# Kernel tuning notes

Measured on AMD Instinct MI355X. Metric: run time of the kernel, lower is better.

The kernel has to match this reference:

```python
import jax, jax.numpy as jnp
import numpy as np

K_BINS = 2048
EMB = 64
MU = 0.99
THRESHOLD = 1.0


def setup_inputs() -> dict:
    key = jax.random.key(0)
    kx, kk = jax.random.split(key)
    x = jax.random.normal(kx, (131072, EMB), dtype=jnp.float32)
    k = jax.random.normal(kk, (K_BINS, EMB), dtype=jnp.float32)
    # restore_k semantics: k_sum starts as a copy of k, k_elem as ones
    return {"x": x, "k": k, "k_sum": k, "k_elem": jnp.ones((K_BINS,), jnp.float32)}


def reference(x, k, k_sum, k_elem):
    N, T = x.shape  # T == EMB (preprocess branch 1)
    # preprocess: prenorm statistic
    prenorm = jnp.linalg.norm(x - jnp.mean(x)) / np.sqrt(x.size)

    # quantise: squared-L2 distance to codebook, argmin, fit
    dist = (jnp.sum(x * x, axis=-1, keepdims=True)
            - 2.0 * (x @ k.T)
            + jnp.sum(k * k, axis=-1)[None, :])  # (N, K_BINS)
    x_l = jnp.argmin(dist, axis=-1)               # (N,)
    fit = jnp.mean(jnp.min(dist, axis=-1))

    # dequantise: codebook gather
    x_d = k[x_l]                                  # (N, EMB)

    # update_k (torch.no_grad block): EMA codebook update
    _k_sum = jax.ops.segment_sum(x, x_l, num_segments=K_BINS)          # == onehot @ x
    _k_elem = jax.ops.segment_sum(jnp.ones((N,), x.dtype), x_l, num_segments=K_BINS)
    # N >= K_BINS so _tile is identity; randperm -> deterministic jax perm
    perm = jax.random.permutation(jax.random.key(42), N)
    _k_rand = x[perm[:K_BINS]]                    # (K_BINS, EMB)
    new_k_sum = MU * k_sum + (1.0 - MU) * _k_sum
    new_k_elem = MU * k_elem + (1.0 - MU) * _k_elem
    usage = (new_k_elem[:, None] >= THRESHOLD).astype(x.dtype)
    new_k = usage * (new_k_sum / new_k_elem[:, None]) + (1.0 - usage) * _k_rand
    _k_prob = _k_elem / jnp.sum(_k_elem)
    entropy = -jnp.sum(_k_prob * jnp.log(_k_prob + 1e-8))
    used_curr = jnp.sum((_k_elem >= THRESHOLD).astype(jnp.int32))
    usage_total = jnp.sum(usage)
    dk = jnp.linalg.norm(new_k - k) / np.sqrt(new_k.size)

    # commit loss (x_d detached) and straight-through estimator
    commit_loss = jnp.sum((jax.lax.stop_gradient(x_d) - x) ** 2) / x.size
    x_d_st = x + jax.lax.stop_gradient(x_d - x)

    # postprocess: view(N, T, -1).permute(0, 2, 1) -> (N, 1, EMB)
    x_d_out = x_d_st.reshape(N, T, -1).transpose(0, 2, 1)
    return (x_l, x_d_out, commit_loss, fit, prenorm,
            entropy, used_curr, usage_total, dk,
            new_k, new_k_sum, new_k_elem)
```

## Files before the change

kernel.cpp:

```cpp
#include <hip/hip_runtime.h>
#include <stdint.h>

#define N_ROWS 131072
#define DIM 64
#define KB 2048
#define M_ELEMS 8388608

#define O_XL   0
#define O_XD   131072
#define O_CL   8519680
#define O_FIT  8519681
#define O_PRE  8519682
#define O_ENT  8519683
#define O_USED 8519684
#define O_UTOT 8519685
#define O_DK   8519686
#define O_NK   8519687
#define O_NKS  8650759
#define O_NKE  8781831

#define A_DBL   0
#define A_CNT   64
#define A_KK2N  128
#define A_KST   8320
#define A_XLI   532608
#define A_KCNT  1056896
#define A_BCUR  1065088
#define A_KRAND 1073280
#define A_BOFF  1597568
#define A_FLAG  1605760
#define A_ROWL  2130048
#define A_KS64  2654336
#define A_BITS  1605760
#define A_PKEY  2130048
#define A_HIST  3702912
#define A_BSUM  3833984
#define A_CUR   3834496
#define A_PIDX  3965568
#define A_RES1  4489856
#define WS_END  5014144

typedef short bf16x8 __attribute__((ext_vector_type(8)));
typedef float f32x4 __attribute__((ext_vector_type(4)));

#define GLL16(G, L) __builtin_amdgcn_global_load_lds( \
    (const __attribute__((address_space(1))) void*)(G), \
    (__attribute__((address_space(3))) void*)(L), 16, 0, 0)
#define GLL4(G, L) __builtin_amdgcn_global_load_lds( \
    (const __attribute__((address_space(1))) void*)(G), \
    (__attribute__((address_space(3))) void*)(L), 4, 0, 0)


__device__ __forceinline__ float block_reduce_sum(float v, float* lds) {
  #pragma unroll
  for (int off = 32; off > 0; off >>= 1) v += __shfl_down(v, off, 64);
  int lane = threadIdx.x & 63, wid = threadIdx.x >> 6;
  if (lane == 0) lds[wid] = v;
  __syncthreads();
  float r = 0.f;
  if (threadIdx.x == 0) {
    int nw = blockDim.x >> 6;
    for (int i = 0; i < nw; ++i) r += lds[i];
  }
  __syncthreads();
  return r;
}

__device__ __forceinline__ unsigned short f2bf_rne(float f) {
  uint32_t u = __float_as_uint(f);
  uint32_t r = u + 0x7FFFu + ((u >> 16) & 1u);
  return (unsigned short)(r >> 16);
}

#define TF_ROUND(r) do { x0 += x1; x1 = (x1 << (r)) | (x1 >> (32 - (r))); x1 ^= x0; } while (0)

__device__ __forceinline__ void threefry2x32(uint32_t k0, uint32_t k1,
                                             uint32_t c0, uint32_t c1,
                                             uint32_t& o0, uint32_t& o1) {
  uint32_t k2 = k0 ^ k1 ^ 0x1BD11BDAu;
  uint32_t x0 = c0 + k0, x1 = c1 + k1;
  TF_ROUND(13); TF_ROUND(15); TF_ROUND(26); TF_ROUND(6);
  x0 += k1; x1 += k2 + 1u;
  TF_ROUND(17); TF_ROUND(29); TF_ROUND(16); TF_ROUND(24);
  x0 += k2; x1 += k0 + 2u;
  TF_ROUND(13); TF_ROUND(15); TF_ROUND(26); TF_ROUND(6);
  x0 += k0; x1 += k1 + 3u;
  TF_ROUND(17); TF_ROUND(29); TF_ROUND(16); TF_ROUND(24);
  x0 += k1; x1 += k2 + 4u;
  TF_ROUND(13); TF_ROUND(15); TF_ROUND(26); TF_ROUND(6);
  x0 += k2; x1 += k0 + 5u;
  o0 = x0; o1 = x1;
}

__global__ __launch_bounds__(256) void k_prep(
    const float* __restrict__ k, unsigned short* __restrict__ kst,
    float* __restrict__ kk2n) {
  int w = (blockIdx.x * blockDim.x + threadIdx.x) >> 6;
  int lane = threadIdx.x & 63;
  float v = k[(size_t)w * DIM + lane];
  unsigned short h = f2bf_rne(v);
  float hf = __uint_as_float((uint32_t)h << 16);
  unsigned short lo = f2bf_rne(v - hf);
  int t = w >> 4, r = w & 15;
  int c = lane >> 3, e = lane & 7;
  int slot = c ^ (r & 7);
  size_t u16i = (size_t)t * 2048 + r * 64 + slot * 8 + e;
  kst[u16i] = h;
  kst[u16i + 1024] = lo;
  float q = v * v;
  #pragma unroll
  for (int off = 32; off > 0; off >>= 1) q += __shfl_down(q, off, 64);
  if (lane == 0) kk2n[w] = -0.5f * q;
}

__global__ __launch_bounds__(512) void k_main(
    const float* __restrict__ x, const unsigned short* __restrict__ kst,
    const float* __restrict__ kk2n,
    int* __restrict__ xli, uint32_t* __restrict__ flag, int* __restrict__ cnt,
    double* __restrict__ dbl) {
  __shared__ __align__(16) char smem[8704];
  __shared__ float lds_red[8];
  int lane = threadIdx.x & 63;
  int wid = threadIdx.x >> 6;
  int lrow = lane & 15;
  int lk = lane >> 4;
  int r0 = (blockIdx.x * 8 + wid) * 32;

  bf16x8 xh[2][2], xl[2][2];
  float s_acc = 0.f, q_acc = 0.f;
  #pragma unroll
  for (int g = 0; g < 2; ++g) {
    #pragma unroll
    for (int kt = 0; kt < 2; ++kt) {
      const float* xp = x + (size_t)(r0 + g * 16 + lrow) * DIM + kt * 32 + lk * 8;
      float4 v0 = *(const float4*)xp;
      float4 v1 = *(const float4*)(xp + 4);
      float vv[8] = {v0.x, v0.y, v0.z, v0.w, v1.x, v1.y, v1.z, v1.w};
      #pragma unroll
      for (int i = 0; i < 8; ++i) {
        float v = vv[i];
        s_acc += v;
        q_acc = fmaf(v, v, q_acc);
        unsigned short h = f2bf_rne(v);
        float hf = __uint_as_float((uint32_t)h << 16);
        xh[g][kt][i] = (short)h;
        xl[g][kt][i] = (short)f2bf_rne(v - hf);
      }
    }
  }
  float bs = block_reduce_sum(s_acc, lds_red);
  float bq = block_reduce_sum(q_acc, lds_red);
  if (threadIdx.x == 0) {
    atomicAdd(&dbl[0], (double)bs);
    atomicAdd(&dbl[1], (double)bq);
  }

  int offH0 = lrow * 128 + (((lk    ) ^ (lrow & 7)) << 4);
  int offH1 = lrow * 128 + (((lk + 4) ^ (lrow & 7)) << 4);

  const char* kst_b = (const char*)kst;
  const char* kk_b  = (const char*)kk2n;

  if (wid < 4) GLL16(kst_b + (size_t)wid * 1024 + (size_t)lane * 16, smem + wid * 1024);
  else if (wid == 4) GLL4(kk_b + (size_t)(lane & 15) * 4, smem + 4096);

  float b1[2], b2[2];
  uint32_t j1[2];
  #pragma unroll
  for (int g = 0; g < 2; ++g) { b1[g] = -3.402823466e38f; b2[g] = -3.402823466e38f; j1[g] = 0; }

  for (int t = 0; t < KB / 16; ++t) {
    char* B  = smem + (t & 1) * 4352;
    char* Bn = smem + ((t + 1) & 1) * 4352;
    if (t + 1 < KB / 16) {
      if (wid < 4)
        GLL16(kst_b + (size_t)(t + 1) * 4096 + (size_t)wid * 1024 + (size_t)lane * 16,
              Bn + wid * 1024);
      else if (wid == 4)
        GLL4(kk_b + (size_t)(t + 1) * 64 + (size_t)(lane & 15) * 4, Bn + 4096);
    }
    __syncthreads();

    bf16x8 ah0 = *(const bf16x8*)(B + offH0);
    bf16x8 ah1 = *(const bf16x8*)(B + offH1);
    bf16x8 al0 = *(const bf16x8*)(B + 2048 + offH0);
    bf16x8 al1 = *(const bf16x8*)(B + 2048 + offH1);
    f32x4 kkv  = *(const f32x4*)(B + 4096 + lk * 16);
    uint32_t jb = (uint32_t)(t * 16 + lk * 4);
    #pragma unroll
    for (int g = 0; g < 2; ++g) {
      f32x4 acc = __builtin_amdgcn_mfma_f32_16x16x32_bf16(ah0, xh[g][0], kkv, 0, 0, 0);
      acc = __builtin_amdgcn_mfma_f32_16x16x32_bf16(ah1, xh[g][1], acc, 0, 0, 0);
      acc = __builtin_amdgcn_mfma_f32_16x16x32_bf16(al0, xh[g][0], acc, 0, 0, 0);
      acc = __builtin_amdgcn_mfma_f32_16x16x32_bf16(al1, xh[g][1], acc, 0, 0, 0);
      acc = __builtin_amdgcn_mfma_f32_16x16x32_bf16(ah0, xl[g][0], acc, 0, 0, 0);
      acc = __builtin_amdgcn_mfma_f32_16x16x32_bf16(ah1, xl[g][1], acc, 0, 0, 0);
      #pragma unroll
      for (int reg = 0; reg < 4; ++reg) {
        float v = acc[reg];
        bool gt = v > b1[g];
        float mn = fminf(v, b1[g]);
        b2[g] = fmaxf(b2[g], mn);
        b1[g] = gt ? v : b1[g];
        j1[g] = gt ? (jb + (uint32_t)reg) : j1[g];
      }
    }
    __syncthreads();
  }

  #pragma unroll
  for (int g = 0; g < 2; ++g) {
    #pragma unroll
    for (int s = 16; s <= 32; s <<= 1) {
      float ob1 = __shfl_xor(b1[g], s, 64);
      float ob2 = __shfl_xor(b2[g], s, 64);
      uint32_t oj1 = __shfl_xor(j1[g], s, 64);
      bool gt = ob1 > b1[g];
      float mn = fminf(b1[g], ob1);
      b2[g] = fmaxf(fmaxf(b2[g], ob2), mn);
      b1[g] = fmaxf(b1[g], ob1);
      j1[g] = gt ? oj1 : j1[g];
    }
    if (lk == 0) {
      int row = r0 + g * 16 + lrow;
      xli[row] = (int)j1[g];
      if (b1[g] - b2[g] < 0.01f) {
        int i = atomicAdd(cnt, 1);
        flag[i] = (uint32_t)row;
      }
    }
  }
}

__global__ __launch_bounds__(256) void k_rescan(
    const uint32_t* __restrict__ flag, const int* __restrict__ cnt,
    const float* __restrict__ x, const float* __restrict__ k,
    int* __restrict__ xli) {
  __shared__ float xs[4][64];
  int lane = threadIdx.x & 63;
  int wid = threadIdx.x >> 6;
  int gw = (blockIdx.x * blockDim.x + threadIdx.x) >> 6;
  int n = *cnt;
  for (int fi = gw; fi < n; fi += 1024) {
    int row = flag[fi];
    xs[wid][lane] = x[(size_t)row * DIM + lane];
    double bd = 1e300;
    int bj = 0;
    for (int j = lane; j < KB; j += 64) {
      const float* kr = k + (size_t)j * DIM;
      double e = 0.0;
      #pragma unroll
      for (int d = 0; d < DIM; ++d) {
        double diff = (double)xs[wid][d] - (double)kr[d];
        e = fma(diff, diff, e);
      }
      if (e < bd) { bd = e; bj = j; }
    }
    #pragma unroll
    for (int off = 32; off > 0; off >>= 1) {
      double od = __shfl_down(bd, off, 64);
      int oj = __shfl_down(bj, off, 64);
      if (od < bd || (od == bd && oj < bj)) { bd = od; bj = oj; }
    }
    if (lane == 0) xli[row] = bj;
  }
}

__global__ void k_hist_rows(const int* __restrict__ xli, int* __restrict__ kcnt) {
  int i = blockIdx.x * blockDim.x + threadIdx.x;
  atomicAdd(&kcnt[xli[i]], 1);
}

__global__ __launch_bounds__(256) void k_finish(
    const float* __restrict__ x, const float* __restrict__ k,
    const int* __restrict__ xli, float* __restrict__ out,
    double* __restrict__ dbl) {
  __shared__ float lds[8];
  int row = blockIdx.x * blockDim.x + threadIdx.x;
  int j = xli[row];
  out[O_XL + row] = (float)j;
  const float4* xp = (const float4*)(x + (size_t)row * DIM);
  const float4* kp = (const float4*)(k + (size_t)j * DIM);
  float4* xd = (float4*)(out + O_XD + (size_t)row * DIM);
  float a = 0.f, b = 0.f, c = 0.f, d = 0.f;
  #pragma unroll
  for (int q = 0; q < 16; ++q) {
    float4 kv = kp[q];
    float4 xv = xp[q];
    xd[q] = kv;
    float dx = kv.x - xv.x, dy = kv.y - xv.y;
    float dz = kv.z - xv.z, dw = kv.w - xv.w;
    a = fmaf(dx, dx, a); b = fmaf(dy, dy, b);
    c = fmaf(dz, dz, c); d = fmaf(dw, dw, d);
  }
  float cl = (a + b) + (c + d);
  float bc = block_reduce_sum(cl, lds);
  if (threadIdx.x == 0) atomicAdd(&dbl[2], (double)bc);
}


__global__ __launch_bounds__(1024) void k_scan_bins(const int* __restrict__ kcnt,
                                                    uint32_t* __restrict__ boffs) {
  __shared__ uint32_t part[1024];
  int tid = threadIdx.x;
  uint32_t c0 = (uint32_t)kcnt[2 * tid];
  uint32_t c1 = (uint32_t)kcnt[2 * tid + 1];
  part[tid] = c0 + c1;
  __syncthreads();
  for (int off = 1; off < 1024; off <<= 1) {
    uint32_t v = (tid >= off) ? part[tid - off] : 0u;
    __syncthreads();
    part[tid] += v;
    __syncthreads();
  }
  uint32_t run = (tid > 0) ? part[tid - 1] : 0u;
  boffs[2 * tid] = run;
  boffs[2 * tid + 1] = run + c0;
}

__global__ void k_scatter_rows(const int* __restrict__ xli, const uint32_t* __restrict__ boffs,
                               uint32_t* __restrict__ bcur, uint32_t* __restrict__ rowlist) {
  int i = blockIdx.x * blockDim.x + threadIdx.x;
  int b = xli[i];
  uint32_t pos = boffs[b] + atomicAdd(&bcur[b], 1u);
  rowlist[pos] = (uint32_t)i;
}

__global__ __launch_bounds__(256) void k_segsum(
    const uint32_t* __restrict__ rowlist, const int* __restrict__ xli,
    const float* __restrict__ x, double* __restrict__ ks64) {
  int gw = (blockIdx.x * blockDim.x + threadIdx.x) >> 6;
  int lane = threadIdx.x & 63;
  uint32_t p0 = (uint32_t)gw * 16;
  double acc = 0.0;
  int cur = -1;
  #pragma unroll 4
  for (int i = 0; i < 16; ++i) {
    uint32_t row = rowlist[p0 + i];
    int bin = xli[row];
    if (bin != cur) {
      if (cur >= 0) atomicAdd(&ks64[(size_t)cur * DIM + lane], acc);
      acc = 0.0; cur = bin;
    }
    acc += (double)x[(size_t)row * DIM + lane];
  }
  if (cur >= 0) atomicAdd(&ks64[(size_t)cur * DIM + lane], acc);
}


__global__ void k_bits_hist(int which, uint32_t* __restrict__ bits,
                            uint32_t* __restrict__ hist) {
  uint32_t a0, a1, b0, b1;
  threefry2x32(0u, 42u, 0u, 2u, a0, b0);
  threefry2x32(0u, 42u, 1u, 3u, a1, b1);
  uint32_t k0, k1;
  if (which == 0) { k0 = b0; k1 = b1; }
  else {
    uint32_t c0, c1, d0, d1;
    threefry2x32(a0, a1, 0u, 2u, c0, d0);
    threefry2x32(a0, a1, 1u, 3u, c1, d1);
    k0 = d0; k1 = d1;
  }
  int i = blockIdx.x * blockDim.x + threadIdx.x;
  uint32_t y0, y1;
  threefry2x32(k0, k1, (uint32_t)i, (uint32_t)(i + 65536), y0, y1);
  bits[i] = y0;
  bits[i + 65536] = y1;
  atomicAdd(&hist[y0 >> 17], 1u);
  atomicAdd(&hist[y1 >> 17], 1u);
}

__global__ __launch_bounds__(256) void k_scanA(uint32_t* __restrict__ hist,
                                               uint32_t* __restrict__ bsum) {
  __shared__ uint32_t sh[256];
  int tid = threadIdx.x;
  int bin = blockIdx.x * 256 + tid;
  uint32_t v = hist[bin];
  sh[tid] = v;
  __syncthreads();
  for (int off = 1; off < 256; off <<= 1) {
    uint32_t t = (tid >= off) ? sh[tid - off] : 0u;
    __syncthreads();
    sh[tid] += t;
    __syncthreads();
  }
  hist[bin] = sh[tid] - v;
  if (tid == 255) bsum[blockIdx.x] = sh[tid];
}

__global__ void k_scanB(uint32_t* __restrict__ bsum) {
  __shared__ uint32_t sh[128];
  int tid = threadIdx.x;
  uint32_t v = bsum[tid];
  sh[tid] = v;
  __syncthreads();
  for (int off = 1; off < 128; off <<= 1) {
    uint32_t t = (tid >= off) ? sh[tid - off] : 0u;
    __syncthreads();
    sh[tid] += t;
    __syncthreads();
  }
  bsum[tid] = sh[tid] - v;
}

__global__ void k_scatter(const uint32_t* __restrict__ bits, const uint32_t* __restrict__ hist,
                          const uint32_t* __restrict__ bsum, uint32_t* __restrict__ cursor,
                          uint32_t* __restrict__ pkey, uint32_t* __restrict__ pidx) {
  int i = blockIdx.x * blockDim.x + threadIdx.x;
  uint32_t key = bits[i];
  uint32_t bin = key >> 17;
  uint32_t pos = hist[bin] + bsum[bin >> 8] + atomicAdd(&cursor[bin], 1u);
  pkey[pos] = key; pidx[pos] = (uint32_t)i;
}

__global__ void k_rank(const uint32_t* __restrict__ pkey, const uint32_t* __restrict__ pidx,
                       const uint32_t* __restrict__ hist, const uint32_t* __restrict__ bsum,
                       const uint32_t* __restrict__ cursor,
                       const uint32_t* __restrict__ srcvals, uint32_t* __restrict__ outv,
                       const float* __restrict__ x, float* __restrict__ krand,
                       int limit) {
  int s = blockIdx.x * blockDim.x + threadIdx.x;
  uint32_t myk = pkey[s], myi = pidx[s];
  uint32_t bin = myk >> 17;
  uint32_t start = hist[bin] + bsum[bin >> 8], cntb = cursor[bin];
  uint32_t r = 0;
  for (uint32_t t = 0; t < cntb; ++t) {
    uint32_t ok = pkey[start + t], oi = pidx[start + t];
    r += (ok < myk || (ok == myk && oi < myi)) ? 1u : 0u;
  }
  uint32_t pos = start + r;
  if (limit == 0) {
    outv[pos] = myi;
  } else if (pos < (uint32_t)limit) {
    uint32_t orig = srcvals[myi];
    const float4* xs = (const float4*)(x + (size_t)orig * DIM);
    float4* kd = (float4*)(krand + (size_t)pos * DIM);
    #pragma unroll
    for (int q = 0; q < 16; ++q) kd[q] = xs[q];
  }
}


__global__ __launch_bounds__(256) void k_elem_kernel(
    const double* __restrict__ ks64, const int* __restrict__ kcnt,
    const float* __restrict__ k_sum_in, const float* __restrict__ k_elem_in,
    const float* __restrict__ k_in, const float* __restrict__ krand,
    float* __restrict__ out, double* __restrict__ dbl) {
  __shared__ float lds[8];
  const float OMF = (float)(1.0 - 0.99);
  int e = blockIdx.x * blockDim.x + threadIdx.x;
  int b = e >> 6;
  float part = (float)ks64[e];
  float nks = 0.99f * k_sum_in[e] + OMF * part;
  out[O_NKS + e] = nks;
  float cnt = (float)kcnt[b];
  float ke = 0.99f * k_elem_in[b] + OMF * cnt;
  float nk = (ke >= 1.f) ? (nks / ke) : krand[e];
  out[O_NK + e] = nk;
  float dd = nk - k_in[e];
  float bsum = block_reduce_sum(dd * dd, lds);
  if (threadIdx.x == 0) atomicAdd(&dbl[4], (double)bsum);
}

__global__ __launch_bounds__(1024) void k_finale(
    const int* __restrict__ kcnt, const float* __restrict__ k_elem_in,
    float* __restrict__ out, const double* __restrict__ dbl) {
  __shared__ float ent_l[1024];
  __shared__ int u1_l[1024], u2_l[1024];
  const float OMF = (float)(1.0 - 0.99);
  int tid = threadIdx.x;
  float ent = 0.f; int used = 0, usage = 0;
  #pragma unroll
  for (int t = 0; t < 2; ++t) {
    int b = tid + t * 1024;
    float cnt = (float)kcnt[b];
    float ke = 0.99f * k_elem_in[b] + OMF * cnt;
    out[O_NKE + b] = ke;
    float p = cnt * (1.f / 131072.f);
    ent -= p * logf(p + 1e-8f);
    used += (cnt >= 1.f) ? 1 : 0;
    usage += (ke >= 1.f) ? 1 : 0;
  }
  ent_l[tid] = ent; u1_l[tid] = used; u2_l[tid] = usage;
  __syncthreads();
  for (int off = 512; off > 0; off >>= 1) {
    if (tid < off) {
      ent_l[tid] += ent_l[tid + off];
      u1_l[tid] += u1_l[tid + off];
      u2_l[tid] += u2_l[tid + off];
    }
    __syncthreads();
  }
  if (tid == 0) {
    double M = (double)M_ELEMS;
    double sumS = dbl[0], sumQ = dbl[1];
    double var = (sumQ - sumS * sumS / M) / M;
    out[O_PRE] = (float)sqrt(var > 0.0 ? var : 0.0);
    out[O_FIT] = (float)(dbl[2] / (double)N_ROWS);
    out[O_CL]  = (float)(dbl[2] / M);
    out[O_DK]  = (float)sqrt(dbl[4] / (double)(KB * DIM));
    out[O_ENT] = ent_l[0];
    out[O_USED] = (float)u1_l[0];
    out[O_UTOT] = (float)u2_l[0];
  }
}


extern "C" void kernel_launch(void* const* d_in, const int* in_sizes, int n_in,
                              void* d_out, int out_size, void* d_ws, size_t ws_size,
                              hipStream_t stream) {
  (void)in_sizes; (void)n_in; (void)out_size; (void)ws_size;
  const float* x      = (const float*)d_in[0];
  const float* k      = (const float*)d_in[1];
  const float* k_sum  = (const float*)d_in[2];
  const float* k_elem = (const float*)d_in[3];
  float* out = (float*)d_out;
  char* ws = (char*)d_ws;

  double*   dbl   = (double*)(ws + A_DBL);
  int*      cnt   = (int*)(ws + A_CNT);
  float*    kk2n  = (float*)(ws + A_KK2N);
  unsigned short* kst = (unsigned short*)(ws + A_KST);
  int*      xli   = (int*)(ws + A_XLI);
  int*      kcnt  = (int*)(ws + A_KCNT);
  uint32_t* bcur  = (uint32_t*)(ws + A_BCUR);
  float*    krand = (float*)(ws + A_KRAND);
  uint32_t* boffs = (uint32_t*)(ws + A_BOFF);
  uint32_t* flag  = (uint32_t*)(ws + A_FLAG);
  uint32_t* rowl  = (uint32_t*)(ws + A_ROWL);
  double*   ks64  = (double*)(ws + A_KS64);
  uint32_t* bits  = (uint32_t*)(ws + A_BITS);
  uint32_t* pkey  = (uint32_t*)(ws + A_PKEY);
  uint32_t* hist  = (uint32_t*)(ws + A_HIST);
  uint32_t* bsum  = (uint32_t*)(ws + A_BSUM);
  uint32_t* cur   = (uint32_t*)(ws + A_CUR);
  uint32_t* pidx  = (uint32_t*)(ws + A_PIDX);
  uint32_t* res1  = (uint32_t*)(ws + A_RES1);

  (void)hipMemsetAsync(ws + A_DBL, 0, 128, stream);
  (void)hipMemsetAsync(ws + A_KCNT, 0, 16384, stream);
  (void)hipMemsetAsync(ws + A_KS64, 0, 1048576, stream);

  k_prep<<<512, 256, 0, stream>>>(k, kst, kk2n);
  k_main<<<512, 512, 0, stream>>>(x, kst, kk2n, xli, flag, cnt, dbl);
  k_rescan<<<256, 256, 0, stream>>>(flag, cnt, x, k, xli);
  k_finish<<<512, 256, 0, stream>>>(x, k, xli, out, dbl);

  k_hist_rows<<<512, 256, 0, stream>>>(xli, kcnt);
  k_scan_bins<<<1, 1024, 0, stream>>>(kcnt, boffs);
  k_scatter_rows<<<512, 256, 0, stream>>>(xli, boffs, bcur, rowl);
  k_segsum<<<2048, 256, 0, stream>>>(rowl, xli, x, ks64);

  (void)hipMemsetAsync(ws + A_HIST, 0, 262656, stream);
  k_bits_hist<<<256, 256, 0, stream>>>(0, bits, hist);
  k_scanA<<<128, 256, 0, stream>>>(hist, bsum);
  k_scanB<<<1, 128, 0, stream>>>(bsum);
  k_scatter<<<512, 256, 0, stream>>>(bits, hist, bsum, cur, pkey, pidx);
  k_rank<<<512, 256, 0, stream>>>(pkey, pidx, hist, bsum, cur, nullptr, res1,
                                  nullptr, nullptr, 0);
  (void)hipMemsetAsync(ws + A_HIST, 0, 262656, stream);
  k_bits_hist<<<256, 256, 0, stream>>>(1, bits, hist);
  k_scanA<<<128, 256, 0, stream>>>(hist, bsum);
  k_scanB<<<1, 128, 0, stream>>>(bsum);
  k_scatter<<<512, 256, 0, stream>>>(bits, hist, bsum, cur, pkey, pidx);
  k_rank<<<512, 256, 0, stream>>>(pkey, pidx, hist, bsum, cur, res1, nullptr,
                                  x, krand, 2048);

  k_elem_kernel<<<512, 256, 0, stream>>>(ks64, kcnt, k_sum, k_elem, k, krand, out, dbl);
  k_finale<<<1, 1024, 0, stream>>>(kcnt, k_elem, out, dbl);
}
```

Measured before the change: 392.5 us.

## Enlarge k_main row tile per wave and stage 64 codebook entries per sync

The main distance/argmin kernel now runs 4 waves of 64 rows each (instead of 8 waves of 32 rows) and loads 64 codebook entries per LDS stage instead of 16. Fewer barriers are needed (one per 64 codes), each LDS fragment read is reused across four row groups, and the work per block stays the same. In exchange each wave holds twice as many x fragments and argmin trackers, which raises register pressure and may lower occupancy. The LDS buffer also grows to about 33KB.

```diff
diff --git a/kernel.cpp b/kernel.cpp
--- a/kernel.cpp
+++ b/kernel.cpp
@@ -113,23 +113,24 @@
   if (lane == 0) kk2n[w] = -0.5f * q;
 }
 
-__global__ __launch_bounds__(512) void k_main(
+__global__ __launch_bounds__(256) void k_main(
     const float* __restrict__ x, const unsigned short* __restrict__ kst,
     const float* __restrict__ kk2n,
     int* __restrict__ xli, uint32_t* __restrict__ flag, int* __restrict__ cnt,
     double* __restrict__ dbl) {
-  __shared__ __align__(16) char smem[8704];
-  __shared__ float lds_red[8];
-  int lane = threadIdx.x & 63;
-  int wid = threadIdx.x >> 6;
+  __shared__ __align__(16) char smem[2][16640];
+  __shared__ float lds_red[4];
+  int tid = threadIdx.x;
+  int lane = tid & 63;
+  int wid = tid >> 6;
   int lrow = lane & 15;
   int lk = lane >> 4;
-  int r0 = (blockIdx.x * 8 + wid) * 32;
-
-  bf16x8 xh[2][2], xl[2][2];
+  int r0 = (blockIdx.x * 4 + wid) * 64;
+
+  bf16x8 xh[4][2], xl[4][2];
   float s_acc = 0.f, q_acc = 0.f;
   #pragma unroll
-  for (int g = 0; g < 2; ++g) {
+  for (int g = 0; g < 4; ++g) {
     #pragma unroll
     for (int kt = 0; kt < 2; ++kt) {
       const float* xp = x + (size_t)(r0 + g * 16 + lrow) * DIM + kt * 32 + lk * 8;
@@ -150,7 +151,7 @@
   }
   float bs = block_reduce_sum(s_acc, lds_red);
   float bq = block_reduce_sum(q_acc, lds_red);
-  if (threadIdx.x == 0) {
+  if (tid == 0) {
     atomicAdd(&dbl[0], (double)bs);
     atomicAdd(&dbl[1], (double)bq);
   }
@@ -161,55 +162,63 @@
   const char* kst_b = (const char*)kst;
   const char* kk_b  = (const char*)kk2n;
 
-  if (wid < 4) GLL16(kst_b + (size_t)wid * 1024 + (size_t)lane * 16, smem + wid * 1024);
-  else if (wid == 4) GLL4(kk_b + (size_t)(lane & 15) * 4, smem + 4096);
-
-  float b1[2], b2[2];
-  uint32_t j1[2];
-  #pragma unroll
-  for (int g = 0; g < 2; ++g) { b1[g] = -3.402823466e38f; b2[g] = -3.402823466e38f; j1[g] = 0; }
-
-  for (int t = 0; t < KB / 16; ++t) {
-    char* B  = smem + (t & 1) * 4352;
-    char* Bn = smem + ((t + 1) & 1) * 4352;
-    if (t + 1 < KB / 16) {
-      if (wid < 4)
-        GLL16(kst_b + (size_t)(t + 1) * 4096 + (size_t)wid * 1024 + (size_t)lane * 16,
-              Bn + wid * 1024);
-      else if (wid == 4)
-        GLL4(kk_b + (size_t)(t + 1) * 64 + (size_t)(lane & 15) * 4, Bn + 4096);
-    }
-    __syncthreads();
-
-    bf16x8 ah0 = *(const bf16x8*)(B + offH0);
-    bf16x8 ah1 = *(const bf16x8*)(B + offH1);
-    bf16x8 al0 = *(const bf16x8*)(B + 2048 + offH0);
-    bf16x8 al1 = *(const bf16x8*)(B + 2048 + offH1);
-    f32x4 kkv  = *(const f32x4*)(B + 4096 + lk * 16);
-    uint32_t jb = (uint32_t)(t * 16 + lk * 4);
+  {
+    char* ldst = &smem[0][0];
     #pragma unroll
-    for (int g = 0; g < 2; ++g) {
-      f32x4 acc = __builtin_amdgcn_mfma_f32_16x16x32_bf16(ah0, xh[g][0], kkv, 0, 0, 0);
-      acc = __builtin_amdgcn_mfma_f32_16x16x32_bf16(ah1, xh[g][1], acc, 0, 0, 0);
-      acc = __builtin_amdgcn_mfma_f32_16x16x32_bf16(al0, xh[g][0], acc, 0, 0, 0);
-      acc = __builtin_amdgcn_mfma_f32_16x16x32_bf16(al1, xh[g][1], acc, 0, 0, 0);
-      acc = __builtin_amdgcn_mfma_f32_16x16x32_bf16(ah0, xl[g][0], acc, 0, 0, 0);
-      acc = __builtin_amdgcn_mfma_f32_16x16x32_bf16(ah1, xl[g][1], acc, 0, 0, 0);
+    for (int c = 0; c < 4; ++c)
+      GLL16(kst_b + c * 4096 + tid * 16, ldst + c * 4096 + tid * 16);
+    if (wid == 0) GLL4(kk_b + lane * 4, ldst + 16384 + lane * 4);
+  }
+
+  float b1[4], b2[4];
+  uint32_t j1[4];
+  #pragma unroll
+  for (int g = 0; g < 4; ++g) {
+    b1[g] = -3.402823466e38f; b2[g] = -3.402823466e38f; j1[g] = 0;
+  }
+
+  for (int t = 0; t < 32; ++t) {
+    __syncthreads();
+    if (t + 1 < 32) {
+      const char* gsrc = kst_b + (size_t)(t + 1) * 16384;
+      char* ldst = &smem[(t + 1) & 1][0];
       #pragma unroll
-      for (int reg = 0; reg < 4; ++reg) {
-        float v = acc[reg];
-        bool gt = v > b1[g];
-        float mn = fminf(v, b1[g]);
-        b2[g] = fmaxf(b2[g], mn);
-        b1[g] = gt ? v : b1[g];
-        j1[g] = gt ? (jb + (uint32_t)reg) : j1[g];
+      for (int c = 0; c < 4; ++c)
+        GLL16(gsrc + c * 4096 + tid * 16, ldst + c * 4096 + tid * 16);
+      if (wid == 0) GLL4(kk_b + (size_t)(t + 1) * 256 + lane * 4, ldst + 16384 + lane * 4);
+    }
+    const char* B = &smem[t & 1][0];
+    #pragma unroll
+    for (int s = 0; s < 4; ++s) {
+      bf16x8 ah0 = *(const bf16x8*)(B + s * 4096 + offH0);
+      bf16x8 ah1 = *(const bf16x8*)(B + s * 4096 + offH1);
+      bf16x8 al0 = *(const bf16x8*)(B + s * 4096 + 2048 + offH0);
+      bf16x8 al1 = *(const bf16x8*)(B + s * 4096 + 2048 + offH1);
+      f32x4 kkv  = *(const f32x4*)(B + 16384 + s * 64 + lk * 16);
+      uint32_t jb = (uint32_t)(t * 64 + s * 16 + lk * 4);
+      #pragma unroll
+      for (int g = 0; g < 4; ++g) {
+        f32x4 acc = __builtin_amdgcn_mfma_f32_16x16x32_bf16(ah0, xh[g][0], kkv, 0, 0, 0);
+        acc = __builtin_amdgcn_mfma_f32_16x16x32_bf16(ah1, xh[g][1], acc, 0, 0, 0);
+        acc = __builtin_amdgcn_mfma_f32_16x16x32_bf16(al0, xh[g][0], acc, 0, 0, 0);
+        acc = __builtin_amdgcn_mfma_f32_16x16x32_bf16(al1, xh[g][1], acc, 0, 0, 0);
+        acc = __builtin_amdgcn_mfma_f32_16x16x32_bf16(ah0, xl[g][0], acc, 0, 0, 0);
+        acc = __builtin_amdgcn_mfma_f32_16x16x32_bf16(ah1, xl[g][1], acc, 0, 0, 0);
+        #pragma unroll
+        for (int reg = 0; reg < 4; ++reg) {
+          float v = acc[reg];
+          bool gt = v > b1[g];
+          float mn = fminf(v, b1[g]);
+          b2[g] = fmaxf(b2[g], mn);
+          b1[g] = gt ? v : b1[g];
+          j1[g] = gt ? (jb + (uint32_t)reg) : j1[g];
+        }
       }
     }
-    __syncthreads();
-  }
-
-  #pragma unroll
-  for (int g = 0; g < 2; ++g) {
+  }
+
+  #pragma unroll
+  for (int g = 0; g < 4; ++g) {
     #pragma unroll
     for (int s = 16; s <= 32; s <<= 1) {
       float ob1 = __shfl_xor(b1[g], s, 64);
@@ -542,7 +551,7 @@
   (void)hipMemsetAsync(ws + A_KS64, 0, 1048576, stream);
 
   k_prep<<<512, 256, 0, stream>>>(k, kst, kk2n);
-  k_main<<<512, 512, 0, stream>>>(x, kst, kk2n, xli, flag, cnt, dbl);
+  k_main<<<512, 256, 0, stream>>>(x, kst, kk2n, xli, flag, cnt, dbl);
   k_rescan<<<256, 256, 0, stream>>>(flag, cnt, x, k, xli);
   k_finish<<<512, 256, 0, stream>>>(x, k, xli, out, dbl);
 
```

Result: no change. 385.3 us (-1.8%).
